# Kernel tuning notes

Hardware: AMD Instinct MI355X
Metric: run time of the kernel (lower is better)

Reference implementation:

```python
import jax, jax.numpy as jnp
import numpy as np

N_HD, N_DEL7, N_AVP, N_AVM = 100, 100, 50, 50
DT = 0.001
KAPPA_PHI, KAPPA_Y = 1.0, 1.0
AV_OFFSET = 0.0
ALPHA_TILDE = 10.0
# alpha used in the leak term inside forward():
ALPHA = ALPHA_TILDE + 0.5 * KAPPA_Y / KAPPA_PHI * 1.0 / (KAPPA_PHI + KAPPA_Y)  # 10.25
W_HD_HD_S = ALPHA_TILDE + 1.0 / (KAPPA_PHI + KAPPA_Y) - AV_OFFSET * KAPPA_Y / (KAPPA_Y + KAPPA_PHI)  # 10.5
W_HD_AV_S = np.sqrt(2.0) * KAPPA_Y / (KAPPA_Y + KAPPA_PHI)  # sqrt(2)/2
W_HD_D7_S = 1.0 / (KAPPA_PHI + KAPPA_Y)  # 0.5
W_AV_HD_S = 1.0
W_D7_HD_S = 1.0
TAU_AV = 0.01
TAU_D7 = 0.001


def _id_matr(x_to, x_from, sig):
    d = np.arccos(np.cos(x_to[:, None] - x_from[None, :]))
    M = np.exp(-0.5 * (d / sig) ** 2) / (np.sqrt(2.0 * np.pi) * sig)
    return M / M.sum(1)[0]


def _build_weights():
    p_hd = np.linspace(-np.pi, np.pi - 2 * np.pi / N_HD, N_HD)
    p_d7 = np.linspace(-np.pi, np.pi - 2 * np.pi / N_DEL7, N_DEL7)
    p_avp = np.linspace(-np.pi, np.pi - 2 * np.pi / N_AVP, N_AVP)
    p_avm = np.linspace(-np.pi, np.pi - 2 * np.pi / N_AVM, N_AVM)
    o, w0, w1 = -0.2, 0.0, 2.0
    W_HD_HD = 2.0 / N_HD * (o + np.maximum(0.0, w0 + w1 * np.cos(p_hd[:, None] - p_hd[None, :])))
    W_HD_AVplus = 2.0 / N_AVP * np.maximum(0.0, np.sin(p_hd[:, None] - p_avp[None, :] + np.pi / 4))
    W_HD_AVminus = 2.0 / N_AVM * np.maximum(0.0, -np.sin(p_hd[:, None] - p_avm[None, :] - np.pi / 4))
    W_AVplus_HD = _id_matr(p_avp, p_hd, 0.3)
    W_AVminus_HD = _id_matr(p_avm, p_hd, 0.3)
    d7w0, d7w1 = 0.5, -0.5
    W_Del7_HD = 2.0 / N_DEL7 * (d7w0 + d7w1 * np.cos(p_d7[:, None] - p_hd[None, :]))
    m0, m1 = 0.1, 0.0
    W_Del7_Del7 = 2.0 / N_DEL7 * (m0 + m1 * np.cos(p_d7[:, None] - p_d7[None, :]))
    j = np.pi / 2 * (1 - 2 * m0) / d7w0
    W_HD_Del7 = -j * _id_matr(p_hd, p_d7, 0.1)
    ws = dict(W_HD_HD=W_HD_HD, W_HD_AVplus=W_HD_AVplus, W_HD_AVminus=W_HD_AVminus,
              W_AVplus_HD=W_AVplus_HD, W_AVminus_HD=W_AVminus_HD,
              W_Del7_HD=W_Del7_HD, W_Del7_Del7=W_Del7_Del7, W_HD_Del7=W_HD_Del7)
    return {k: jnp.asarray(v, dtype=jnp.float32) for k, v in ws.items()}


def setup_inputs() -> dict:
    key = jax.random.key(0)
    k1, k2 = jax.random.split(key)
    B, S = 64, 5000
    inp = {
        'inputs': jax.random.normal(k1, (B, S, 2), dtype=jnp.float32),
        'r0': jax.random.uniform(k2, (1, B, N_HD + N_AVP + N_AVM + N_DEL7), dtype=jnp.float32),
    }
    inp.update(_build_weights())
    return inp


def reference(inputs, r0, W_HD_HD, W_HD_AVplus, W_HD_AVminus, W_AVplus_HD,
              W_AVminus_HD, W_Del7_HD, W_Del7_Del7, W_HD_Del7):
    # batch_first -> [seq, batch, 2]
    x = jnp.transpose(inputs, (1, 0, 2))
    r_HD0 = r0[0, :, :N_HD]
    r_AVp0 = r0[0, :, N_HD:N_HD + N_AVP]
    r_AVm0 = r0[0, :, N_HD + N_AVP:N_HD + N_AVP + N_AVM]
    r_D70 = r0[0, :, N_HD + N_AVP + N_AVM:]
    relu = jax.nn.relu

    def step(carry, x_t):
        r_HD, r_AVp, r_AVm, r_D7 = carry
        av = x_t[:, 1]  # [B]; HD input only feeds a dead input_term in the original
        r_HD_new = (r_HD
                    - ALPHA * r_HD * DT
                    + W_HD_HD_S * jnp.einsum('ij,bj->bi', W_HD_HD, r_HD) * DT
                    + W_HD_AV_S * jnp.einsum('ij,bj->bi', W_HD_AVplus, r_AVp) * DT
                    + W_HD_AV_S * jnp.einsum('ij,bj->bi', W_HD_AVminus, r_AVm) * DT
                    + W_HD_D7_S * jnp.einsum('ij,bj->bi', W_HD_Del7, relu(r_D7)) * r_HD * DT)
        gate_p = (av / DT + AV_OFFSET)[:, None]
        gate_m = (-av / DT + AV_OFFSET)[:, None]
        r_AVp_new = r_AVp + (1.0 / TAU_AV) * (-r_AVp + gate_p * W_AV_HD_S * jnp.einsum('ij,bj->bi', W_AVplus_HD, r_HD_new)) * DT
        r_AVm_new = r_AVm + (1.0 / TAU_AV) * (-r_AVm + gate_m * W_AV_HD_S * jnp.einsum('ij,bj->bi', W_AVminus_HD, r_HD_new)) * DT
        r_D7_new = r_D7 + (1.0 / TAU_D7) * (-r_D7
                                            + W_D7_HD_S * jnp.einsum('ij,bj->bi', W_Del7_HD, relu(r_HD_new))
                                            + jnp.einsum('ij,bj->bi', W_Del7_Del7, relu(r_D7))) * DT
        out = jnp.concatenate([r_HD_new, r_AVp_new, r_AVm_new, r_D7_new], axis=1)  # [B, 300]
        return (r_HD_new, r_AVp_new, r_AVm_new, r_D7_new), out

    carry, ys = jax.lax.scan(step, (r_HD0, r_AVp0, r_AVm0, r_D70), x)
    output = jnp.transpose(ys, (1, 0, 2))  # [B, S, 300] (batch_first)
    r_full_curr = jnp.concatenate(carry, axis=1)
    return output, r_full_curr
```

## Files before the change

### kernel.cpp

```cpp
#include <hip/hip_runtime.h>


#define SSTEPS 5000
#define PI_D 3.14159265358979323846

typedef float f2 __attribute__((ext_vector_type(2)));

__device__ __forceinline__ f2 pk_fma(f2 a, f2 b, f2 c) {
  f2 d;
  asm("v_pk_fma_f32 %0, %1, %2, %3" : "=v"(d) : "v"(a), "v"(b), "v"(c));
  return d;
}

template<int CTRL, int RM, bool BC>
__device__ __forceinline__ float dpp_mov_f(float x) {
  return __int_as_float(__builtin_amdgcn_update_dpp(0, __float_as_int(x), CTRL, RM, 0xF, BC));
}
__device__ __forceinline__ float scan16(float x) {
  x += dpp_mov_f<0x111,0xF,true>(x);
  x += dpp_mov_f<0x112,0xF,true>(x);
  x += dpp_mov_f<0x114,0xF,true>(x);
  x += dpp_mov_f<0x118,0xF,true>(x);
  return x;
}
__device__ __forceinline__ float scan8(float x) {
  x += dpp_mov_f<0x111,0xF,true>(x);
  x += dpp_mov_f<0x112,0xF,true>(x);
  x += dpp_mov_f<0x114,0xF,true>(x);
  return x;
}
__device__ __forceinline__ float wave_sum(float x) {
  x = scan16(x);
  x += dpp_mov_f<0x142,0xA,false>(x);
  x += dpp_mov_f<0x143,0xC,false>(x);
  return __int_as_float(__builtin_amdgcn_readlane(__float_as_int(x), 63));
}

__device__ __forceinline__ void bar_lgkm() {
  asm volatile("s_waitcnt lgkmcnt(0)\n\ts_barrier" ::: "memory");
}

__global__ __launch_bounds__(1024, 4) void drosoph_rnn_kernel(
    const float* __restrict__ xin,
    const float* __restrict__ r0,
    const float* __restrict__ W_HD_HD,
    const float* __restrict__ W_HD_AVp,
    const float* __restrict__ W_HD_AVm,
    const float* __restrict__ W_AVp_HD,
    const float* __restrict__ W_AVm_HD,
    const float* __restrict__ W_D7_HD,
    const float* __restrict__ W_D7_D7,
    const float* __restrict__ W_HD_D7,
    float* __restrict__ out)
{
  const int b    = blockIdx.x;
  const int t    = threadIdx.x;

  __shared__ __align__(16) float su[2][328];
  __shared__ float avb[SSTEPS];
  __shared__ float d7r[104];

  const bool p1  = (t < 800);
  const int  g   = t >> 4;
  const int  r1  = t & 15;
  const bool pav = (t < 400);
  const int  a   = t >> 3;
  const int  qa  = t & 7;
  const bool pd7 = (t >= 832) && (t < 960);
  const int  dl  = t & 63;
  const int  o7  = t - 832;
  const bool pst = (t >= 960);

  f2 w1p[2][10];
  if (p1) {
    #pragma unroll
    for (int k = 0; k < 2; ++k) {
      const int o = g + 50*k;
      #pragma unroll
      for (int q = 0; q < 20; ++q) {
        const int j = 20*r1 + q;
        float w;
        if      (j < 100) w = 10.5f                * W_HD_HD [o*100 + j];
        else if (j < 150) w = 0.70710678118654752f * W_HD_AVp[o*50 + (j-100)];
        else if (j < 200) w = 0.70710678118654752f * W_HD_AVm[o*50 + (j-150)];
        else if (j < 300) w = 0.5f                 * W_HD_D7 [o*100 + (j-200)];
        else w = 0.0f;
        w1p[k][q >> 1][q & 1] = w;
      }
    }
  }

  f2 wavp[8];
  if (pav) {
    #pragma unroll
    for (int u = 0; u < 4; ++u) {
      const int j0 = 4*(qa + 8*u);
      #pragma unroll
      for (int m = 0; m < 4; ++m) {
        const int j = j0 + m;
        float w = (j < 100) ? W_AVp_HD[a*100 + j] : 0.0f;
        wavp[2*u + (m >> 1)][m & 1] = w;
      }
    }
  }

  float cw0=0.f, cw1=0.f, sw0=0.f, sw1=0.f, m0w=0.f, m1w=0.f, cd=0.f, sd=0.f;
  if (pd7) {
    const int j0 = 2*dl, j1 = 2*dl + 1;
    double pj0 = -PI_D + j0*(2.0*PI_D/100.0);
    double pj1 = -PI_D + j1*(2.0*PI_D/100.0);
    m0w = (j0 < 100) ? 1.0f : 0.0f;
    m1w = (j1 < 100) ? 1.0f : 0.0f;
    cw0 = m0w * (float)cos(pj0);  sw0 = m0w * (float)sin(pj0);
    cw1 = m1w * (float)cos(pj1);  sw1 = m1w * (float)sin(pj1);
    double po = -PI_D + o7*(2.0*PI_D/100.0);
    cd = (float)cos(po);  sd = (float)sin(po);
  }

  if (t < 328) { su[0][t] = 0.f; su[1][t] = 0.f; }
  if (t < 104) d7r[t] = 0.f;
  {
    const float2* x2 = (const float2*)xin + (size_t)b * SSTEPS;
    for (int i = t; i < SSTEPS; i += 1024) avb[i] = x2[i].y;
  }
  if (t < 300) {
    float v = r0[b*300 + t];
    su[0][t] = (t < 200) ? v : fmaxf(v, 0.f);
  }
  __syncthreads();

  float* outb = out + (size_t)b * ((size_t)SSTEPS * 300);
  int p = 0;

  #pragma unroll 1
  for (int s = 0; s < SSTEPS; ++s) {
    const float* suc = su[p];
    float*       sun = su[p^1];

    if (p1) {
      f2 vv2[10];
      {
        const float4* vp = (const float4*)(suc + 20*r1);
        float4 V0=vp[0], V1=vp[1], V2=vp[2], V3=vp[3], V4=vp[4];
        vv2[0] = f2{V0.x, V0.y}; vv2[1] = f2{V0.z, V0.w};
        vv2[2] = f2{V1.x, V1.y}; vv2[3] = f2{V1.z, V1.w};
        vv2[4] = f2{V2.x, V2.y}; vv2[5] = f2{V2.z, V2.w};
        vv2[6] = f2{V3.x, V3.y}; vv2[7] = f2{V3.z, V3.w};
        vv2[8] = f2{V4.x, V4.y}; vv2[9] = f2{V4.z, V4.w};
      }
      float hd0 = suc[g], hd1 = suc[g+50];
      f2 a0 = f2{0.f,0.f}, b0 = f2{0.f,0.f};
      f2 a1 = f2{0.f,0.f}, b1 = f2{0.f,0.f};
      #pragma unroll
      for (int q2 = 0; q2 < 10; q2 += 2) {
        a0 = pk_fma(w1p[0][q2],   vv2[q2],   a0);
        b0 = pk_fma(w1p[0][q2+1], vv2[q2+1], b0);
        a1 = pk_fma(w1p[1][q2],   vv2[q2],   a1);
        b1 = pk_fma(w1p[1][q2+1], vv2[q2+1], b1);
      }
      float e0 = (a0[0] + a0[1]) + (b0[0] + b0[1]);
      float e1 = (a1[0] + a1[1]) + (b1[0] + b1[1]);
      if (r1 >= 10) { e0 *= hd0; e1 *= hd1; }
      e0 = scan16(e0);
      e1 = scan16(e1);
      if (r1 == 15) {
        float h0 = fmaf(0.001f, fmaf(-10.25f, hd0, e0), hd0);
        float h1 = fmaf(0.001f, fmaf(-10.25f, hd1, e1), hd1);
        sun[g]    = h0;
        sun[g+50] = h1;
      }
    } else if (pst) {
      if (s > 0) {
        float* od = outb + (size_t)(s-1) * 300;
        #pragma unroll
        for (int u = 0; u < 5; ++u) {
          int idx = dl + 64*u;
          if (idx < 300) od[idx] = (idx < 200) ? suc[idx] : d7r[idx-200];
        }
      }
    }
    float T0loc = 0.f;
    if (pd7) {
      float x = 0.f;
      if (dl < 50) { float2 z = *(const float2*)(suc + 200 + 2*dl); x = z.x + z.y; }
      T0loc = wave_sum(x);
    }
    bar_lgkm();

    if (pav) {
      const float4* hp = (const float4*)sun;
      float4 H0 = hp[qa], H1 = hp[qa+8], H2 = hp[qa+16], H3 = hp[qa+24];
      f2 hh2[8];
      hh2[0] = f2{H0.x, H0.y}; hh2[1] = f2{H0.z, H0.w};
      hh2[2] = f2{H1.x, H1.y}; hh2[3] = f2{H1.z, H1.w};
      hh2[4] = f2{H2.x, H2.y}; hh2[5] = f2{H2.z, H2.w};
      hh2[6] = f2{H3.x, H3.y}; hh2[7] = f2{H3.z, H3.w};
      f2 d0 = f2{0.f,0.f}, d1 = f2{0.f,0.f};
      #pragma unroll
      for (int u = 0; u < 8; u += 2) {
        d0 = pk_fma(wavp[u],   hh2[u],   d0);
        d1 = pk_fma(wavp[u+1], hh2[u+1], d1);
      }
      float d = scan8((d0[0] + d0[1]) + (d1[0] + d1[1]));
      if (qa == 7) {
        float av   = avb[s];
        float gp   = av * 1000.0f;
        float oldp = suc[100+a], oldm = suc[150+a];
        float np_  = fmaf(0.1f, fmaf(gp,  d, -oldp), oldp);
        float nm_  = fmaf(0.1f, fmaf(-gp, d, -oldm), oldm);
        sun[100+a] = np_;
        sun[150+a] = nm_;
      }
    }

    if (pd7) {
      float2 y2 = *(const float2*)(sun + 2*dl);
      float y0 = fmaxf(y2.x, 0.f), y1 = fmaxf(y2.y, 0.f);
      float pS0 = fmaf(m1w, y1,   m0w * y0);
      float pC  = fmaf(cw1, y1,   cw0 * y0);
      float pS  = fmaf(sw1, y1,   sw0 * y0);
      float S0 = wave_sum(pS0);
      float C  = wave_sum(pC);
      float S  = wave_sum(pS);
      if (o7 < 100) {
        float d7 = fmaf(0.002f, T0loc, 0.01f * (S0 - fmaf(cd, C, sd * S)));
        sun[200+o7] = fmaxf(d7, 0.f);
        d7r[o7]     = d7;
      }
    }
    bar_lgkm();
    p ^= 1;
  }

  if (t < 300) {
    float v = (t < 200) ? su[p][t] : d7r[t-200];
    outb[(size_t)(SSTEPS-1) * 300 + t] = v;
    out[(size_t)64 * SSTEPS * 300 + (size_t)b * 300 + t] = v;
  }
}

extern "C" void kernel_launch(void* const* d_in, const int* in_sizes, int n_in,
                              void* d_out, int out_size, void* d_ws, size_t ws_size,
                              hipStream_t stream) {
  drosoph_rnn_kernel<<<64, 1024, 0, stream>>>(
      (const float*)d_in[0],
      (const float*)d_in[1],
      (const float*)d_in[2],
      (const float*)d_in[3],
      (const float*)d_in[4],
      (const float*)d_in[5],
      (const float*)d_in[6],
      (const float*)d_in[7],
      (const float*)d_in[8],
      (const float*)d_in[9],
      (float*)d_out);
}
```

Baseline: 3.886 ms.

## Repack per-step work into fewer waves with more outputs per thread

The HD matvec now runs on 400 threads, each computing four output rows instead of two. The AV stage uses 200 threads, each computing two AV outputs. The Del7 stage is folded into a single wave that computes all 100 outputs, two per lane. Cutting the active thread count should reduce per-step barrier cost and wave scheduling overhead in this serial 5000-step loop, at the cost of longer per-thread dependency chains and more registers per thread.

```diff
diff --git a/kernel.cpp b/kernel.cpp
--- a/kernel.cpp
+++ b/kernel.cpp
@@ -35,7 +35,6 @@
   x += dpp_mov_f<0x143,0xC,false>(x);
   return __int_as_float(__builtin_amdgcn_readlane(__float_as_int(x), 63));
 }
-
 __device__ __forceinline__ void bar_lgkm() {
   asm volatile("s_waitcnt lgkmcnt(0)\n\ts_barrier" ::: "memory");
 }
@@ -55,27 +54,27 @@
 {
   const int b    = blockIdx.x;
   const int t    = threadIdx.x;
+  const int lane = t & 63;
+  const int wid  = t >> 6;
 
   __shared__ __align__(16) float su[2][328];
   __shared__ float avb[SSTEPS];
   __shared__ float d7r[104];
 
-  const bool p1  = (t < 800);
+  const bool p1  = (t < 400);
   const int  g   = t >> 4;
   const int  r1  = t & 15;
-  const bool pav = (t < 400);
-  const int  a   = t >> 3;
+  const bool w7  = (wid == 7);
+  const bool pst = (wid == 8);
+  const bool pav = (t >= 512) && (t < 712);
+  const int  ai  = (t - 512) >> 3;
   const int  qa  = t & 7;
-  const bool pd7 = (t >= 832) && (t < 960);
-  const int  dl  = t & 63;
-  const int  o7  = t - 832;
-  const bool pst = (t >= 960);
-
-  f2 w1p[2][10];
+
+  f2 w1p[4][10];
   if (p1) {
     #pragma unroll
-    for (int k = 0; k < 2; ++k) {
-      const int o = g + 50*k;
+    for (int k = 0; k < 4; ++k) {
+      const int o = g + 25*k;
       #pragma unroll
       for (int q = 0; q < 20; ++q) {
         const int j = 20*r1 + q;
@@ -90,31 +89,38 @@
     }
   }
 
-  f2 wavp[8];
+  f2 wavK[2][8];
   if (pav) {
     #pragma unroll
-    for (int u = 0; u < 4; ++u) {
-      const int j0 = 4*(qa + 8*u);
-      #pragma unroll
-      for (int m = 0; m < 4; ++m) {
-        const int j = j0 + m;
-        float w = (j < 100) ? W_AVp_HD[a*100 + j] : 0.0f;
-        wavp[2*u + (m >> 1)][m & 1] = w;
-      }
-    }
-  }
-
-  float cw0=0.f, cw1=0.f, sw0=0.f, sw1=0.f, m0w=0.f, m1w=0.f, cd=0.f, sd=0.f;
-  if (pd7) {
-    const int j0 = 2*dl, j1 = 2*dl + 1;
+    for (int m = 0; m < 2; ++m) {
+      const int a2 = ai + 25*m;
+      #pragma unroll
+      for (int u = 0; u < 4; ++u) {
+        const int j0 = 4*(qa + 8*u);
+        #pragma unroll
+        for (int mm = 0; mm < 4; ++mm) {
+          const int j = j0 + mm;
+          float w = (j < 100) ? W_AVp_HD[a2*100 + j] : 0.0f;
+          wavK[m][2*u + (mm >> 1)][mm & 1] = w;
+        }
+      }
+    }
+  }
+
+  float cw0=0.f, cw1=0.f, sw0=0.f, sw1=0.f, m0w=0.f, m1w=0.f;
+  float cdA=0.f, sdA=0.f, cdB=0.f, sdB=0.f;
+  if (w7) {
+    const int j0 = 2*lane, j1 = 2*lane + 1;
+    m0w = (j0 < 100) ? 1.0f : 0.0f;
+    m1w = (j1 < 100) ? 1.0f : 0.0f;
     double pj0 = -PI_D + j0*(2.0*PI_D/100.0);
     double pj1 = -PI_D + j1*(2.0*PI_D/100.0);
-    m0w = (j0 < 100) ? 1.0f : 0.0f;
-    m1w = (j1 < 100) ? 1.0f : 0.0f;
-    cw0 = m0w * (float)cos(pj0);  sw0 = m0w * (float)sin(pj0);
-    cw1 = m1w * (float)cos(pj1);  sw1 = m1w * (float)sin(pj1);
-    double po = -PI_D + o7*(2.0*PI_D/100.0);
-    cd = (float)cos(po);  sd = (float)sin(po);
+    cw0 = m0w*(float)cos(pj0);  sw0 = m0w*(float)sin(pj0);
+    cw1 = m1w*(float)cos(pj1);  sw1 = m1w*(float)sin(pj1);
+    double pA = -PI_D + lane     *(2.0*PI_D/100.0);
+    double pB = -PI_D + (lane+64)*(2.0*PI_D/100.0);
+    cdA = (float)cos(pA); sdA = (float)sin(pA);
+    cdB = (float)cos(pB); sdB = (float)sin(pB);
   }
 
   if (t < 328) { su[0][t] = 0.f; su[1][t] = 0.f; }
@@ -136,6 +142,7 @@
   for (int s = 0; s < SSTEPS; ++s) {
     const float* suc = su[p];
     float*       sun = su[p^1];
+    float T0loc = 0.f;
 
     if (p1) {
       f2 vv2[10];
@@ -148,42 +155,39 @@
         vv2[6] = f2{V3.x, V3.y}; vv2[7] = f2{V3.z, V3.w};
         vv2[8] = f2{V4.x, V4.y}; vv2[9] = f2{V4.z, V4.w};
       }
-      float hd0 = suc[g], hd1 = suc[g+50];
-      f2 a0 = f2{0.f,0.f}, b0 = f2{0.f,0.f};
-      f2 a1 = f2{0.f,0.f}, b1 = f2{0.f,0.f};
-      #pragma unroll
-      for (int q2 = 0; q2 < 10; q2 += 2) {
-        a0 = pk_fma(w1p[0][q2],   vv2[q2],   a0);
-        b0 = pk_fma(w1p[0][q2+1], vv2[q2+1], b0);
-        a1 = pk_fma(w1p[1][q2],   vv2[q2],   a1);
-        b1 = pk_fma(w1p[1][q2+1], vv2[q2+1], b1);
-      }
-      float e0 = (a0[0] + a0[1]) + (b0[0] + b0[1]);
-      float e1 = (a1[0] + a1[1]) + (b1[0] + b1[1]);
-      if (r1 >= 10) { e0 *= hd0; e1 *= hd1; }
-      e0 = scan16(e0);
-      e1 = scan16(e1);
+      const float hd0 = suc[g],    hd1 = suc[g+25];
+      const float hd2 = suc[g+50], hd3 = suc[g+75];
+      f2 c0={0.f,0.f}, c1={0.f,0.f}, c2={0.f,0.f}, c3={0.f,0.f};
+      #pragma unroll
+      for (int q2 = 0; q2 < 10; ++q2) {
+        c0 = pk_fma(w1p[0][q2], vv2[q2], c0);
+        c1 = pk_fma(w1p[1][q2], vv2[q2], c1);
+        c2 = pk_fma(w1p[2][q2], vv2[q2], c2);
+        c3 = pk_fma(w1p[3][q2], vv2[q2], c3);
+      }
+      float e0 = c0[0]+c0[1], e1 = c1[0]+c1[1];
+      float e2 = c2[0]+c2[1], e3 = c3[0]+c3[1];
+      if (r1 >= 10) { e0 *= hd0; e1 *= hd1; e2 *= hd2; e3 *= hd3; }
+      e0 = scan16(e0); e1 = scan16(e1); e2 = scan16(e2); e3 = scan16(e3);
       if (r1 == 15) {
-        float h0 = fmaf(0.001f, fmaf(-10.25f, hd0, e0), hd0);
-        float h1 = fmaf(0.001f, fmaf(-10.25f, hd1, e1), hd1);
-        sun[g]    = h0;
-        sun[g+50] = h1;
-      }
+        sun[g]    = fmaf(0.001f, fmaf(-10.25f, hd0, e0), hd0);
+        sun[g+25] = fmaf(0.001f, fmaf(-10.25f, hd1, e1), hd1);
+        sun[g+50] = fmaf(0.001f, fmaf(-10.25f, hd2, e2), hd2);
+        sun[g+75] = fmaf(0.001f, fmaf(-10.25f, hd3, e3), hd3);
+      }
+    } else if (w7) {
+      float x = 0.f;
+      if (lane < 50) { float2 z = *(const float2*)(suc + 200 + 2*lane); x = z.x + z.y; }
+      T0loc = wave_sum(x);
     } else if (pst) {
       if (s > 0) {
         float* od = outb + (size_t)(s-1) * 300;
         #pragma unroll
         for (int u = 0; u < 5; ++u) {
-          int idx = dl + 64*u;
+          int idx = lane + 64*u;
           if (idx < 300) od[idx] = (idx < 200) ? suc[idx] : d7r[idx-200];
         }
       }
-    }
-    float T0loc = 0.f;
-    if (pd7) {
-      float x = 0.f;
-      if (dl < 50) { float2 z = *(const float2*)(suc + 200 + 2*dl); x = z.x + z.y; }
-      T0loc = wave_sum(x);
     }
     bar_lgkm();
 
@@ -197,35 +201,44 @@
       hh2[6] = f2{H3.x, H3.y}; hh2[7] = f2{H3.z, H3.w};
       f2 d0 = f2{0.f,0.f}, d1 = f2{0.f,0.f};
       #pragma unroll
-      for (int u = 0; u < 8; u += 2) {
-        d0 = pk_fma(wavp[u],   hh2[u],   d0);
-        d1 = pk_fma(wavp[u+1], hh2[u+1], d1);
-      }
-      float d = scan8((d0[0] + d0[1]) + (d1[0] + d1[1]));
+      for (int u = 0; u < 8; ++u) {
+        d0 = pk_fma(wavK[0][u], hh2[u], d0);
+        d1 = pk_fma(wavK[1][u], hh2[u], d1);
+      }
+      float s0v = scan8(d0[0] + d0[1]);
+      float s1v = scan8(d1[0] + d1[1]);
       if (qa == 7) {
-        float av   = avb[s];
-        float gp   = av * 1000.0f;
-        float oldp = suc[100+a], oldm = suc[150+a];
-        float np_  = fmaf(0.1f, fmaf(gp,  d, -oldp), oldp);
-        float nm_  = fmaf(0.1f, fmaf(-gp, d, -oldm), oldm);
-        sun[100+a] = np_;
-        sun[150+a] = nm_;
-      }
-    }
-
-    if (pd7) {
-      float2 y2 = *(const float2*)(sun + 2*dl);
+        const float gp = avb[s] * 1000.0f;
+        {
+          float oldp = suc[100+ai], oldm = suc[150+ai];
+          sun[100+ai] = fmaf(0.1f, fmaf(gp,  s0v, -oldp), oldp);
+          sun[150+ai] = fmaf(0.1f, fmaf(-gp, s0v, -oldm), oldm);
+        }
+        {
+          float oldp = suc[125+ai], oldm = suc[175+ai];
+          sun[125+ai] = fmaf(0.1f, fmaf(gp,  s1v, -oldp), oldp);
+          sun[175+ai] = fmaf(0.1f, fmaf(-gp, s1v, -oldm), oldm);
+        }
+      }
+    } else if (w7) {
+      float2 y2 = *(const float2*)(sun + 2*lane);
       float y0 = fmaxf(y2.x, 0.f), y1 = fmaxf(y2.y, 0.f);
-      float pS0 = fmaf(m1w, y1,   m0w * y0);
-      float pC  = fmaf(cw1, y1,   cw0 * y0);
-      float pS  = fmaf(sw1, y1,   sw0 * y0);
+      float pS0 = fmaf(m1w, y1, m0w * y0);
+      float pC  = fmaf(cw1, y1, cw0 * y0);
+      float pS  = fmaf(sw1, y1, sw0 * y0);
       float S0 = wave_sum(pS0);
       float C  = wave_sum(pC);
       float S  = wave_sum(pS);
-      if (o7 < 100) {
-        float d7 = fmaf(0.002f, T0loc, 0.01f * (S0 - fmaf(cd, C, sd * S)));
-        sun[200+o7] = fmaxf(d7, 0.f);
-        d7r[o7]     = d7;
+      float base = fmaf(0.002f, T0loc, 0.01f * S0);
+      {
+        float d7 = base - 0.01f * fmaf(cdA, C, sdA * S);
+        sun[200+lane] = fmaxf(d7, 0.f);
+        d7r[lane]     = d7;
+      }
+      if (lane < 36) {
+        float d7 = base - 0.01f * fmaf(cdB, C, sdB * S);
+        sun[264+lane] = fmaxf(d7, 0.f);
+        d7r[64+lane]  = d7;
       }
     }
     bar_lgkm();
```

After: 14.50 ms. 3.73x slower.

## Fuse Del7 cosine reductions into HD stage via per-wave partials

Applied to the files above, without the earlier changes.

The Del7 input sums (sum, cosine and sine projections of relu(r_HD_new)) are now computed by the HD-update threads right after they produce new HD values. Each of those waves reduces its partials and writes them to a small shared buffer before the first barrier. After that barrier one wave only has to combine 13 partials per quantity and write the Del7 outputs as float2. This moves three full wave reductions off the critical path between the two barriers and drops one idle wave (block size 960). It adds DPP reductions to the HD waves and a shared-buffer round trip in exchange.

```diff
diff --git a/kernel.cpp b/kernel.cpp
--- a/kernel.cpp
+++ b/kernel.cpp
@@ -35,12 +35,14 @@
   x += dpp_mov_f<0x143,0xC,false>(x);
   return __int_as_float(__builtin_amdgcn_readlane(__float_as_int(x), 63));
 }
-
+__device__ __forceinline__ float bcast_lane(float x, int l) {
+  return __int_as_float(__builtin_amdgcn_readlane(__float_as_int(x), l));
+}
 __device__ __forceinline__ void bar_lgkm() {
   asm volatile("s_waitcnt lgkmcnt(0)\n\ts_barrier" ::: "memory");
 }
 
-__global__ __launch_bounds__(1024, 4) void drosoph_rnn_kernel(
+__global__ __launch_bounds__(960, 4) void drosoph_rnn_kernel(
     const float* __restrict__ xin,
     const float* __restrict__ r0,
     const float* __restrict__ W_HD_HD,
@@ -55,10 +57,13 @@
 {
   const int b    = blockIdx.x;
   const int t    = threadIdx.x;
+  const int lane = t & 63;
+  const int wid  = t >> 6;
 
   __shared__ __align__(16) float su[2][328];
   __shared__ float avb[SSTEPS];
   __shared__ float d7r[104];
+  __shared__ float pbuf[64];
 
   const bool p1  = (t < 800);
   const int  g   = t >> 4;
@@ -66,10 +71,8 @@
   const bool pav = (t < 400);
   const int  a   = t >> 3;
   const int  qa  = t & 7;
-  const bool pd7 = (t >= 832) && (t < 960);
-  const int  dl  = t & 63;
-  const int  o7  = t - 832;
-  const bool pst = (t >= 960);
+  const bool d7w = (wid == 13);
+  const bool pst = (wid == 14);
 
   f2 w1p[2][10];
   if (p1) {
@@ -104,24 +107,25 @@
     }
   }
 
-  float cw0=0.f, cw1=0.f, sw0=0.f, sw1=0.f, m0w=0.f, m1w=0.f, cd=0.f, sd=0.f;
-  if (pd7) {
-    const int j0 = 2*dl, j1 = 2*dl + 1;
-    double pj0 = -PI_D + j0*(2.0*PI_D/100.0);
-    double pj1 = -PI_D + j1*(2.0*PI_D/100.0);
-    m0w = (j0 < 100) ? 1.0f : 0.0f;
-    m1w = (j1 < 100) ? 1.0f : 0.0f;
-    cw0 = m0w * (float)cos(pj0);  sw0 = m0w * (float)sin(pj0);
-    cw1 = m1w * (float)cos(pj1);  sw1 = m1w * (float)sin(pj1);
-    double po = -PI_D + o7*(2.0*PI_D/100.0);
-    cd = (float)cos(po);  sd = (float)sin(po);
+  float cg = 0.f, sg = 0.f;
+  if (p1 && r1 == 15) {
+    double pg = -PI_D + g * (2.0*PI_D/100.0);
+    cg = (float)cos(pg); sg = (float)sin(pg);
+  }
+  float cdA=0.f, sdA=0.f, cdB=0.f, sdB=0.f;
+  if (d7w) {
+    double pa = -PI_D + (2*lane)  *(2.0*PI_D/100.0);
+    double pb = -PI_D + (2*lane+1)*(2.0*PI_D/100.0);
+    cdA = (float)cos(pa); sdA = (float)sin(pa);
+    cdB = (float)cos(pb); sdB = (float)sin(pb);
   }
 
   if (t < 328) { su[0][t] = 0.f; su[1][t] = 0.f; }
   if (t < 104) d7r[t] = 0.f;
+  if (t < 64)  pbuf[t] = 0.f;
   {
     const float2* x2 = (const float2*)xin + (size_t)b * SSTEPS;
-    for (int i = t; i < SSTEPS; i += 1024) avb[i] = x2[i].y;
+    for (int i = t; i < SSTEPS; i += 960) avb[i] = x2[i].y;
   }
   if (t < 300) {
     float v = r0[b*300 + t];
@@ -136,6 +140,8 @@
   for (int s = 0; s < SSTEPS; ++s) {
     const float* suc = su[p];
     float*       sun = su[p^1];
+    float T0loc = 0.f;
+    float q0 = 0.f, q1 = 0.f, q2 = 0.f;
 
     if (p1) {
       f2 vv2[10];
@@ -152,11 +158,11 @@
       f2 a0 = f2{0.f,0.f}, b0 = f2{0.f,0.f};
       f2 a1 = f2{0.f,0.f}, b1 = f2{0.f,0.f};
       #pragma unroll
-      for (int q2 = 0; q2 < 10; q2 += 2) {
-        a0 = pk_fma(w1p[0][q2],   vv2[q2],   a0);
-        b0 = pk_fma(w1p[0][q2+1], vv2[q2+1], b0);
-        a1 = pk_fma(w1p[1][q2],   vv2[q2],   a1);
-        b1 = pk_fma(w1p[1][q2+1], vv2[q2+1], b1);
+      for (int q = 0; q < 10; q += 2) {
+        a0 = pk_fma(w1p[0][q],   vv2[q],   a0);
+        b0 = pk_fma(w1p[0][q+1], vv2[q+1], b0);
+        a1 = pk_fma(w1p[1][q],   vv2[q],   a1);
+        b1 = pk_fma(w1p[1][q+1], vv2[q+1], b1);
       }
       float e0 = (a0[0] + a0[1]) + (b0[0] + b0[1]);
       float e1 = (a1[0] + a1[1]) + (b1[0] + b1[1]);
@@ -168,22 +174,38 @@
         float h1 = fmaf(0.001f, fmaf(-10.25f, hd1, e1), hd1);
         sun[g]    = h0;
         sun[g+50] = h1;
-      }
+        float rh0 = fmaxf(h0, 0.f), rh1 = fmaxf(h1, 0.f);
+        q0 = rh0 + rh1;
+        float dr = rh0 - rh1;
+        q1 = cg * dr;
+        q2 = sg * dr;
+      }
+    } else if (d7w) {
+      float x = 0.f;
+      if (lane < 50) { float2 z = *(const float2*)(suc + 200 + 2*lane); x = z.x + z.y; }
+      T0loc = wave_sum(x);
     } else if (pst) {
       if (s > 0) {
         float* od = outb + (size_t)(s-1) * 300;
         #pragma unroll
         for (int u = 0; u < 5; ++u) {
-          int idx = dl + 64*u;
+          int idx = lane + 64*u;
           if (idx < 300) od[idx] = (idx < 200) ? suc[idx] : d7r[idx-200];
         }
       }
     }
-    float T0loc = 0.f;
-    if (pd7) {
-      float x = 0.f;
-      if (dl < 50) { float2 z = *(const float2*)(suc + 200 + 2*dl); x = z.x + z.y; }
-      T0loc = wave_sum(x);
+    if (t < 832) {
+      q0 += dpp_mov_f<0x142,0xA,false>(q0);
+      q1 += dpp_mov_f<0x142,0xA,false>(q1);
+      q2 += dpp_mov_f<0x142,0xA,false>(q2);
+      q0 += dpp_mov_f<0x143,0xC,false>(q0);
+      q1 += dpp_mov_f<0x143,0xC,false>(q1);
+      q2 += dpp_mov_f<0x143,0xC,false>(q2);
+      if (lane == 63) {
+        pbuf[wid]      = q0;
+        pbuf[16 + wid] = q1;
+        pbuf[32 + wid] = q2;
+      }
     }
     bar_lgkm();
 
@@ -211,21 +233,18 @@
         sun[100+a] = np_;
         sun[150+a] = nm_;
       }
-    }
-
-    if (pd7) {
-      float2 y2 = *(const float2*)(sun + 2*dl);
-      float y0 = fmaxf(y2.x, 0.f), y1 = fmaxf(y2.y, 0.f);
-      float pS0 = fmaf(m1w, y1,   m0w * y0);
-      float pC  = fmaf(cw1, y1,   cw0 * y0);
-      float pS  = fmaf(sw1, y1,   sw0 * y0);
-      float S0 = wave_sum(pS0);
-      float C  = wave_sum(pC);
-      float S  = wave_sum(pS);
-      if (o7 < 100) {
-        float d7 = fmaf(0.002f, T0loc, 0.01f * (S0 - fmaf(cd, C, sd * S)));
-        sun[200+o7] = fmaxf(d7, 0.f);
-        d7r[o7]     = d7;
+    } else if (d7w) {
+      float v = pbuf[lane];
+      v = scan16(v);
+      float S0 = bcast_lane(v, 15);
+      float C  = bcast_lane(v, 31);
+      float S  = bcast_lane(v, 47);
+      float base = fmaf(0.002f, T0loc, 0.01f * S0);
+      if (lane < 50) {
+        float da = base - 0.01f * fmaf(cdA, C, sdA * S);
+        float db = base - 0.01f * fmaf(cdB, C, sdB * S);
+        *(float2*)(sun + 200 + 2*lane) = make_float2(fmaxf(da, 0.f), fmaxf(db, 0.f));
+        *(float2*)(d7r + 2*lane)       = make_float2(da, db);
       }
     }
     bar_lgkm();
@@ -242,7 +261,7 @@
 extern "C" void kernel_launch(void* const* d_in, const int* in_sizes, int n_in,
                               void* d_out, int out_size, void* d_ws, size_t ws_size,
                               hipStream_t stream) {
-  drosoph_rnn_kernel<<<64, 1024, 0, stream>>>(
+  drosoph_rnn_kernel<<<64, 960, 0, stream>>>(
       (const float*)d_in[0],
       (const float*)d_in[1],
       (const float*)d_in[2],
```

New measurement: 4.652 ms. 19.7% more time.
